# Performance work log

Measured on AMD Instinct MI355X. Metric: run time of the kernel, lower is better.

The kernel has to match this reference:

```python
import jax, jax.numpy as jnp
import numpy as np

B, N_RIGIDS, N_RES = 16, 8192, 2048
C_FRAME, C_S, N_AA = 384, 384, 21
EPS = 1e-5


def setup_inputs() -> dict:
    key = jax.random.key(0)
    ks = jax.random.split(key, 8)
    rigids_embed_flat = jax.random.normal(ks[0], (B, N_RIGIDS, C_FRAME), dtype=jnp.float32)
    rigids_to_res_idx = jax.random.randint(ks[1], (B, N_RIGIDS), 0, N_RES, dtype=jnp.int64)
    rigids_mask = jnp.ones((B, N_RIGIDS), dtype=jnp.float32)
    out = jax.random.normal(ks[2], (B, N_RES, C_S), dtype=jnp.float32)
    # params
    ln_g = jnp.ones((C_FRAME,), dtype=jnp.float32)
    ln_b = jnp.zeros((C_FRAME,), dtype=jnp.float32)
    W_su = jax.random.normal(ks[3], (C_FRAME, C_S), dtype=jnp.float32) / np.sqrt(C_FRAME)
    b_su = jnp.zeros((C_S,), dtype=jnp.float32)
    W_out = jax.random.normal(ks[4], (C_S, N_AA), dtype=jnp.float32) / np.sqrt(C_S)
    b_out = jnp.zeros((N_AA,), dtype=jnp.float32)
    return {
        "rigids_embed_flat": rigids_embed_flat,
        "rigids_to_res_idx": rigids_to_res_idx,
        "rigids_mask": rigids_mask,
        "out": out,
        "ln_g": ln_g, "ln_b": ln_b,
        "W_su": W_su, "b_su": b_su,
        "W_out": W_out, "b_out": b_out,
    }


def _layernorm(x, g, b):
    mu = jnp.mean(x, axis=-1, keepdims=True)
    var = jnp.mean(jnp.square(x - mu), axis=-1, keepdims=True)
    return (x - mu) * jax.lax.rsqrt(var + EPS) * g + b


def reference(rigids_embed_flat, rigids_to_res_idx, rigids_mask, out,
              ln_g, ln_b, W_su, b_su, W_out, b_out):
    # 1) LayerNorm over frame channel dim
    x = _layernorm(rigids_embed_flat, ln_g, ln_b)            # [B, N_rigids, c_frame]
    # 2) project frame embed -> c_s and mask invalid frames
    y = (jnp.einsum("bnf,fs->bns", x, W_su) + b_su) * rigids_mask[..., None]
    # 3) scatter-add masked frame contributions into per-residue slots
    seq_embed = jax.vmap(lambda o, yy, ii: o.at[ii].add(yy))(out, y, rigids_to_res_idx)  # [B, N_res, c_s]
    # 4) final projection to amino-acid logits
    return jnp.einsum("brs,sa->bra", seq_embed, W_out) + b_out  # [B, N_res, n_aa]
```

## Files before the change

### kernel.cpp

```cpp
#include <hip/hip_runtime.h>

#define BATCH 16
#define N_RIGIDS 8192
#define N_RES 2048
#define C_FRAME 384
#define C_S 384
#define N_AA 21
#define EPS 1e-5f

#define N_RIG_TOT (BATCH * N_RIGIDS)
#define N_ROWS    (BATCH * N_RES)
#define CAP 32
#define ZROW 32

#define GC_OFF 0
#define CS_OFF 8192
#define B2_OFF 8256
#define HIST_OFF 16384
#define ZB_OFF 65536

__global__ void __launch_bounds__(384) precompute_fused(const float* __restrict__ W_su,
                                                        const float* __restrict__ W_out,
                                                        const float* __restrict__ ln_g,
                                                        const float* __restrict__ ln_b,
                                                        const float* __restrict__ b_su,
                                                        float* __restrict__ ws) {
    __shared__ float sg[6], sb[6];
    const int a = blockIdx.x;
    const int f = threadIdx.x;
    const float4* wrow = (const float4*)(W_su + (size_t)f * C_S);
    float wc = 0.f;
    for (int j = 0; j < C_S / 4; ++j) {
        float4 v = wrow[j];
        wc += v.x * W_out[(4 * j + 0) * N_AA + a];
        wc += v.y * W_out[(4 * j + 1) * N_AA + a];
        wc += v.z * W_out[(4 * j + 2) * N_AA + a];
        wc += v.w * W_out[(4 * j + 3) * N_AA + a];
    }
    float gval = ln_g[f] * wc;
    ws[GC_OFF + f * N_AA + a] = gval;
    float bval = ln_b[f] * wc + b_su[f] * W_out[f * N_AA + a];
    float g = gval, b = bval;
#pragma unroll
    for (int off = 32; off >= 1; off >>= 1) {
        g += __shfl_xor(g, off);
        b += __shfl_xor(b, off);
    }
    int lane = f & 63, w = f >> 6;
    if (lane == 0) { sg[w] = g; sb[w] = b; }
    __syncthreads();
    if (f == 0) {
        float cs = 0.f, b2 = 0.f;
#pragma unroll
        for (int i = 0; i < 6; ++i) { cs += sg[i]; b2 += sb[i]; }
        ws[CS_OFF + a] = cs;
        ws[B2_OFF + a] = b2;
    }
}

__global__ void __launch_bounds__(128) zcompute(const float* __restrict__ embed,
                                                const int* __restrict__ idx,
                                                const float* __restrict__ mask,
                                                const float* __restrict__ ws,
                                                float* __restrict__ zb,
                                                int* __restrict__ hist) {
    __shared__ float lds[2][128 * 33];
    const int tid = threadIdx.x;
    const int t = blockIdx.x * 128 + tid;
    const float* __restrict__ Gc = ws + GC_OFF;
    const float4* gb = (const float4*)(embed + (size_t)blockIdx.x * (128 * C_FRAME));
    float4 buf[8];
    float d[N_AA];
#pragma unroll
    for (int a = 0; a < N_AA; ++a) d[a] = 0.f;
    float sum = 0.f, sumsq = 0.f;

#pragma unroll
    for (int k = 0; k < 8; ++k) {
        int f4 = tid + 128 * k;
        buf[k] = gb[(f4 >> 3) * 96 + (f4 & 7)];
    }
#pragma unroll
    for (int k = 0; k < 8; ++k) {
        int f4 = tid + 128 * k;
        float* p = &lds[0][(f4 >> 3) * 33 + (f4 & 7) * 4];
        p[0] = buf[k].x; p[1] = buf[k].y; p[2] = buf[k].z; p[3] = buf[k].w;
    }
    __syncthreads();

    for (int c = 0; c < 12; ++c) {
        if (c + 1 < 12) {
            const float4* gn = gb + (c + 1) * 8;
#pragma unroll
            for (int k = 0; k < 8; ++k) {
                int f4 = tid + 128 * k;
                buf[k] = gn[(f4 >> 3) * 96 + (f4 & 7)];
            }
        }
        const float* row = &lds[c & 1][tid * 33];
        const float* g = Gc + (c * 32) * N_AA;
#pragma unroll 4
        for (int cc = 0; cc < 32; ++cc) {
            float x = row[cc];
            sum += x; sumsq += x * x;
#pragma unroll
            for (int a = 0; a < N_AA; ++a) d[a] += x * g[cc * N_AA + a];
        }
        if (c + 1 < 12) {
#pragma unroll
            for (int k = 0; k < 8; ++k) {
                int f4 = tid + 128 * k;
                float* p = &lds[(c + 1) & 1][(f4 >> 3) * 33 + (f4 & 7) * 4];
                p[0] = buf[k].x; p[1] = buf[k].y; p[2] = buf[k].z; p[3] = buf[k].w;
            }
            __syncthreads();
        }
    }

    float mu  = sum * (1.f / C_FRAME);
    float var = sumsq * (1.f / C_FRAME) - mu * mu;
    float inv = rsqrtf(var + EPS);
    float m = mask[t];
    int res = idx[t];
    int b = t >> 13;
    int g = (b << 11) + res;
    const float* cs = ws + CS_OFF;
    const float* b2 = ws + B2_OFF;
    float v[N_AA];
#pragma unroll
    for (int a = 0; a < N_AA; ++a) v[a] = m * (inv * (d[a] - mu * cs[a]) + b2[a]);
    int slot = atomicAdd(hist + g, 1);
    if (slot < CAP) {
        float4* zr = (float4*)(zb + ((size_t)g * CAP + slot) * ZROW);
        zr[0] = make_float4(v[0], v[1], v[2], v[3]);
        zr[1] = make_float4(v[4], v[5], v[6], v[7]);
        zr[2] = make_float4(v[8], v[9], v[10], v[11]);
        zr[3] = make_float4(v[12], v[13], v[14], v[15]);
        zr[4] = make_float4(v[16], v[17], v[18], v[19]);
        ((float*)zr)[20] = v[20];
    }
}

__global__ void __launch_bounds__(128) final_gather(const float* __restrict__ out_in,
                                                    const float* __restrict__ W_out,
                                                    const float* __restrict__ b_out,
                                                    const float* __restrict__ zb,
                                                    const int* __restrict__ hist,
                                                    float* __restrict__ logits) {
    __shared__ float lds[2][128 * 33];
    const int tid = threadIdx.x;
    const int gidx = blockIdx.x * 128 + tid;
    const float4* gb = (const float4*)(out_in + (size_t)blockIdx.x * (128 * C_S));
    float4 buf[8];
    float acc[N_AA];
#pragma unroll
    for (int a = 0; a < N_AA; ++a) acc[a] = b_out[a];

#pragma unroll
    for (int k = 0; k < 8; ++k) {
        int f4 = tid + 128 * k;
        buf[k] = gb[(f4 >> 3) * 96 + (f4 & 7)];
    }
#pragma unroll
    for (int k = 0; k < 8; ++k) {
        int f4 = tid + 128 * k;
        float* p = &lds[0][(f4 >> 3) * 33 + (f4 & 7) * 4];
        p[0] = buf[k].x; p[1] = buf[k].y; p[2] = buf[k].z; p[3] = buf[k].w;
    }
    __syncthreads();

    for (int c = 0; c < 12; ++c) {
        if (c + 1 < 12) {
            const float4* gn = gb + (c + 1) * 8;
#pragma unroll
            for (int k = 0; k < 8; ++k) {
                int f4 = tid + 128 * k;
                buf[k] = gn[(f4 >> 3) * 96 + (f4 & 7)];
            }
        }
        const float* row = &lds[c & 1][tid * 33];
        const float* w = W_out + (c * 32) * N_AA;
#pragma unroll 4
        for (int cc = 0; cc < 32; ++cc) {
            float x = row[cc];
#pragma unroll
            for (int a = 0; a < N_AA; ++a) acc[a] += x * w[cc * N_AA + a];
        }
        if (c + 1 < 12) {
#pragma unroll
            for (int k = 0; k < 8; ++k) {
                int f4 = tid + 128 * k;
                float* p = &lds[(c + 1) & 1][(f4 >> 3) * 33 + (f4 & 7) * 4];
                p[0] = buf[k].x; p[1] = buf[k].y; p[2] = buf[k].z; p[3] = buf[k].w;
            }
            __syncthreads();
        }
    }

    int cnt = hist[gidx];
    if (cnt > CAP) cnt = CAP;
    const float* zbase = zb + (size_t)gidx * CAP * ZROW;
    for (int i = 0; i < cnt; ++i) {
        const float4* zr = (const float4*)(zbase + i * ZROW);
        float4 z0 = zr[0], z1 = zr[1], z2 = zr[2], z3 = zr[3], z4 = zr[4];
        float  z5 = ((const float*)zr)[20];
        acc[0] += z0.x; acc[1] += z0.y; acc[2] += z0.z; acc[3] += z0.w;
        acc[4] += z1.x; acc[5] += z1.y; acc[6] += z1.z; acc[7] += z1.w;
        acc[8] += z2.x; acc[9] += z2.y; acc[10] += z2.z; acc[11] += z2.w;
        acc[12] += z3.x; acc[13] += z3.y; acc[14] += z3.z; acc[15] += z3.w;
        acc[16] += z4.x; acc[17] += z4.y; acc[18] += z4.z; acc[19] += z4.w;
        acc[20] += z5;
    }
    float* o = logits + (size_t)gidx * N_AA;
#pragma unroll
    for (int a = 0; a < N_AA; ++a) o[a] = acc[a];
}

extern "C" void kernel_launch(void* const* d_in, const int* in_sizes, int n_in,
                              void* d_out, int out_size, void* d_ws, size_t ws_size,
                              hipStream_t stream) {
    const float* embed  = (const float*)d_in[0];
    const int*   idx    = (const int*)d_in[1];
    const float* mask   = (const float*)d_in[2];
    const float* out_in = (const float*)d_in[3];
    const float* ln_g   = (const float*)d_in[4];
    const float* ln_b   = (const float*)d_in[5];
    const float* W_su   = (const float*)d_in[6];
    const float* b_su   = (const float*)d_in[7];
    const float* W_out  = (const float*)d_in[8];
    const float* b_out  = (const float*)d_in[9];
    float* logits = (float*)d_out;
    float* ws = (float*)d_ws;
    float* zb   = ws + ZB_OFF;
    int*   hist = (int*)(ws + HIST_OFF);

    hipMemsetAsync(hist, 0, N_ROWS * sizeof(int), stream);
    hipLaunchKernelGGL(precompute_fused, dim3(N_AA), dim3(384), 0, stream,
                       W_su, W_out, ln_g, ln_b, b_su, ws);
    hipLaunchKernelGGL(zcompute, dim3(N_RIG_TOT / 128), dim3(128), 0, stream,
                       embed, idx, mask, ws, zb, hist);
    hipLaunchKernelGGL(final_gather, dim3(N_ROWS / 128), dim3(128), 0, stream,
                       out_in, W_out, b_out, zb, hist, logits);
}
```

Measured before the change: 429.8 us.

## Split final_gather rows across four threads and pad W_out for vector loads

The final gather kernel now assigns four threads per residue row, each handling a quarter of the channel chunk, and combines partial sums with lane shuffles. Blocks now cover 32 rows instead of 128, so there are four times as many. W_out is copied into a 24-wide padded layout in the workspace so the inner loop can load it as float4. The precompute kernel is also split into 64-thread blocks that combine partial sums with atomics, which needs an extra memset. The aim is more parallelism and occupancy in the final stage, at the cost of shuffle reductions and a strided gather of the scatter buffer.

```diff
diff --git a/kernel.cpp b/kernel.cpp
--- a/kernel.cpp
+++ b/kernel.cpp
@@ -6,6 +6,7 @@
 #define C_FRAME 384
 #define C_S 384
 #define N_AA 21
+#define N_AA_PAD 24
 #define EPS 1e-5f
 
 #define N_RIG_TOT (BATCH * N_RIGIDS)
@@ -16,18 +17,26 @@
 #define GC_OFF 0
 #define CS_OFF 8192
 #define B2_OFF 8256
-#define HIST_OFF 16384
+#define WP_OFF 8320
+#define HIST_OFF 18432
 #define ZB_OFF 65536
 
-__global__ void __launch_bounds__(384) precompute_fused(const float* __restrict__ W_su,
-                                                        const float* __restrict__ W_out,
-                                                        const float* __restrict__ ln_g,
-                                                        const float* __restrict__ ln_b,
-                                                        const float* __restrict__ b_su,
-                                                        float* __restrict__ ws) {
-    __shared__ float sg[6], sb[6];
-    const int a = blockIdx.x;
-    const int f = threadIdx.x;
+__global__ void __launch_bounds__(64) precompute_fused(const float* __restrict__ W_su,
+                                                       const float* __restrict__ W_out,
+                                                       const float* __restrict__ ln_g,
+                                                       const float* __restrict__ ln_b,
+                                                       const float* __restrict__ b_su,
+                                                       float* __restrict__ ws) {
+    const int f = blockIdx.x * 64 + threadIdx.x;
+    if (blockIdx.y == N_AA) {
+        float* wp = ws + WP_OFF + (size_t)f * N_AA_PAD;
+        const float* wo = W_out + (size_t)f * N_AA;
+#pragma unroll
+        for (int a = 0; a < N_AA; ++a) wp[a] = wo[a];
+        wp[21] = 0.f; wp[22] = 0.f; wp[23] = 0.f;
+        return;
+    }
+    const int a = blockIdx.y;
     const float4* wrow = (const float4*)(W_su + (size_t)f * C_S);
     float wc = 0.f;
     for (int j = 0; j < C_S / 4; ++j) {
@@ -46,15 +55,9 @@
         g += __shfl_xor(g, off);
         b += __shfl_xor(b, off);
     }
-    int lane = f & 63, w = f >> 6;
-    if (lane == 0) { sg[w] = g; sb[w] = b; }
-    __syncthreads();
-    if (f == 0) {
-        float cs = 0.f, b2 = 0.f;
-#pragma unroll
-        for (int i = 0; i < 6; ++i) { cs += sg[i]; b2 += sb[i]; }
-        ws[CS_OFF + a] = cs;
-        ws[B2_OFF + a] = b2;
+    if (threadIdx.x == 0) {
+        atomicAdd(ws + CS_OFF + a, g);
+        atomicAdd(ws + B2_OFF + a, b);
     }
 }
 
@@ -142,27 +145,30 @@
 }
 
 __global__ void __launch_bounds__(128) final_gather(const float* __restrict__ out_in,
-                                                    const float* __restrict__ W_out,
                                                     const float* __restrict__ b_out,
+                                                    const float* __restrict__ ws,
                                                     const float* __restrict__ zb,
                                                     const int* __restrict__ hist,
                                                     float* __restrict__ logits) {
-    __shared__ float lds[2][128 * 33];
+    __shared__ float lds[2][32 * 33];
     const int tid = threadIdx.x;
-    const int gidx = blockIdx.x * 128 + tid;
-    const float4* gb = (const float4*)(out_in + (size_t)blockIdx.x * (128 * C_S));
-    float4 buf[8];
-    float acc[N_AA];
-#pragma unroll
-    for (int a = 0; a < N_AA; ++a) acc[a] = b_out[a];
-
-#pragma unroll
-    for (int k = 0; k < 8; ++k) {
+    const int r = tid >> 2;
+    const int ks = tid & 3;
+    const int gidx = blockIdx.x * 32 + r;
+    const float* __restrict__ Wp = ws + WP_OFF;
+    const float4* gb = (const float4*)(out_in + (size_t)blockIdx.x * (32 * C_S));
+    float4 buf[2];
+    float acc[N_AA_PAD];
+#pragma unroll
+    for (int a = 0; a < N_AA_PAD; ++a) acc[a] = 0.f;
+
+#pragma unroll
+    for (int k = 0; k < 2; ++k) {
         int f4 = tid + 128 * k;
         buf[k] = gb[(f4 >> 3) * 96 + (f4 & 7)];
     }
 #pragma unroll
-    for (int k = 0; k < 8; ++k) {
+    for (int k = 0; k < 2; ++k) {
         int f4 = tid + 128 * k;
         float* p = &lds[0][(f4 >> 3) * 33 + (f4 & 7) * 4];
         p[0] = buf[k].x; p[1] = buf[k].y; p[2] = buf[k].z; p[3] = buf[k].w;
@@ -173,22 +179,28 @@
         if (c + 1 < 12) {
             const float4* gn = gb + (c + 1) * 8;
 #pragma unroll
-            for (int k = 0; k < 8; ++k) {
+            for (int k = 0; k < 2; ++k) {
                 int f4 = tid + 128 * k;
                 buf[k] = gn[(f4 >> 3) * 96 + (f4 & 7)];
             }
         }
-        const float* row = &lds[c & 1][tid * 33];
-        const float* w = W_out + (c * 32) * N_AA;
-#pragma unroll 4
-        for (int cc = 0; cc < 32; ++cc) {
+        const float* row = &lds[c & 1][r * 33 + ks * 8];
+        const float4* w4 = (const float4*)(Wp + (size_t)(c * 32 + ks * 8) * N_AA_PAD);
+#pragma unroll
+        for (int cc = 0; cc < 8; ++cc) {
             float x = row[cc];
 #pragma unroll
-            for (int a = 0; a < N_AA; ++a) acc[a] += x * w[cc * N_AA + a];
-        }
-        if (c + 1 < 12) {
-#pragma unroll
-            for (int k = 0; k < 8; ++k) {
+            for (int q = 0; q < 6; ++q) {
+                float4 wv = w4[cc * 6 + q];
+                acc[4 * q + 0] += x * wv.x;
+                acc[4 * q + 1] += x * wv.y;
+                acc[4 * q + 2] += x * wv.z;
+                acc[4 * q + 3] += x * wv.w;
+            }
+        }
+        if (c + 1 < 12) {
+#pragma unroll
+            for (int k = 0; k < 2; ++k) {
                 int f4 = tid + 128 * k;
                 float* p = &lds[(c + 1) & 1][(f4 >> 3) * 33 + (f4 & 7) * 4];
                 p[0] = buf[k].x; p[1] = buf[k].y; p[2] = buf[k].z; p[3] = buf[k].w;
@@ -200,20 +212,16 @@
     int cnt = hist[gidx];
     if (cnt > CAP) cnt = CAP;
     const float* zbase = zb + (size_t)gidx * CAP * ZROW;
-    for (int i = 0; i < cnt; ++i) {
-        const float4* zr = (const float4*)(zbase + i * ZROW);
-        float4 z0 = zr[0], z1 = zr[1], z2 = zr[2], z3 = zr[3], z4 = zr[4];
-        float  z5 = ((const float*)zr)[20];
-        acc[0] += z0.x; acc[1] += z0.y; acc[2] += z0.z; acc[3] += z0.w;
-        acc[4] += z1.x; acc[5] += z1.y; acc[6] += z1.z; acc[7] += z1.w;
-        acc[8] += z2.x; acc[9] += z2.y; acc[10] += z2.z; acc[11] += z2.w;
-        acc[12] += z3.x; acc[13] += z3.y; acc[14] += z3.z; acc[15] += z3.w;
-        acc[16] += z4.x; acc[17] += z4.y; acc[18] += z4.z; acc[19] += z4.w;
-        acc[20] += z5;
-    }
     float* o = logits + (size_t)gidx * N_AA;
 #pragma unroll
-    for (int a = 0; a < N_AA; ++a) o[a] = acc[a];
+    for (int a = 0; a < N_AA; ++a) {
+        float t = acc[a];
+        if (ks == 0) t += b_out[a];
+        for (int i = ks; i < cnt; i += 4) t += zbase[i * ZROW + a];
+        t += __shfl_xor(t, 1);
+        t += __shfl_xor(t, 2);
+        if (ks == 0) o[a] = t;
+    }
 }
 
 extern "C" void kernel_launch(void* const* d_in, const int* in_sizes, int n_in,
@@ -235,10 +243,11 @@
     int*   hist = (int*)(ws + HIST_OFF);
 
     hipMemsetAsync(hist, 0, N_ROWS * sizeof(int), stream);
-    hipLaunchKernelGGL(precompute_fused, dim3(N_AA), dim3(384), 0, stream,
+    hipMemsetAsync(ws + CS_OFF, 0, (B2_OFF - CS_OFF + N_AA) * sizeof(float), stream);
+    hipLaunchKernelGGL(precompute_fused, dim3(6, N_AA + 1), dim3(64), 0, stream,
                        W_su, W_out, ln_g, ln_b, b_su, ws);
     hipLaunchKernelGGL(zcompute, dim3(N_RIG_TOT / 128), dim3(128), 0, stream,
                        embed, idx, mask, ws, zb, hist);
-    hipLaunchKernelGGL(final_gather, dim3(N_ROWS / 128), dim3(128), 0, stream,
-                       out_in, W_out, b_out, zb, hist, logits);
-}
+    hipLaunchKernelGGL(final_gather, dim3(N_ROWS / 32), dim3(128), 0, stream,
+                       out_in, b_out, ws, zb, hist, logits);
+}
```

After: 499.3 us. +16.2%, slower.

## Split final_gather channel reduction across waves and parallelize precompute over blocks

Applied to the files above, without the earlier changes.

final_gather now assigns 64 rows per block and has four waves each handle a quarter of the c_s channels, reducing partial logits through LDS. The scatter-bucket gather is then spread over four threads per row, each covering a strided subset of output columns. precompute_fused spreads each amino-acid column over six 64-thread blocks and combines the partial sums with atomics into a zero-initialized buffer. This raises parallelism in both kernels, at the cost of an extra memset, float atomics and more barriers, and with fewer rows per block the number of blocks doubles.

```diff
diff --git a/kernel.cpp b/kernel.cpp
--- a/kernel.cpp
+++ b/kernel.cpp
@@ -16,18 +16,17 @@
 #define GC_OFF 0
 #define CS_OFF 8192
 #define B2_OFF 8256
-#define HIST_OFF 16384
+#define HIST_OFF 18432
 #define ZB_OFF 65536
 
-__global__ void __launch_bounds__(384) precompute_fused(const float* __restrict__ W_su,
-                                                        const float* __restrict__ W_out,
-                                                        const float* __restrict__ ln_g,
-                                                        const float* __restrict__ ln_b,
-                                                        const float* __restrict__ b_su,
-                                                        float* __restrict__ ws) {
-    __shared__ float sg[6], sb[6];
-    const int a = blockIdx.x;
-    const int f = threadIdx.x;
+__global__ void __launch_bounds__(64) precompute_fused(const float* __restrict__ W_su,
+                                                       const float* __restrict__ W_out,
+                                                       const float* __restrict__ ln_g,
+                                                       const float* __restrict__ ln_b,
+                                                       const float* __restrict__ b_su,
+                                                       float* __restrict__ ws) {
+    const int f = blockIdx.x * 64 + threadIdx.x;
+    const int a = blockIdx.y;
     const float4* wrow = (const float4*)(W_su + (size_t)f * C_S);
     float wc = 0.f;
     for (int j = 0; j < C_S / 4; ++j) {
@@ -46,15 +45,9 @@
         g += __shfl_xor(g, off);
         b += __shfl_xor(b, off);
     }
-    int lane = f & 63, w = f >> 6;
-    if (lane == 0) { sg[w] = g; sb[w] = b; }
-    __syncthreads();
-    if (f == 0) {
-        float cs = 0.f, b2 = 0.f;
-#pragma unroll
-        for (int i = 0; i < 6; ++i) { cs += sg[i]; b2 += sb[i]; }
-        ws[CS_OFF + a] = cs;
-        ws[B2_OFF + a] = b2;
+    if (threadIdx.x == 0) {
+        atomicAdd(ws + CS_OFF + a, g);
+        atomicAdd(ws + B2_OFF + a, b);
     }
 }
 
@@ -141,79 +134,86 @@
     }
 }
 
-__global__ void __launch_bounds__(128) final_gather(const float* __restrict__ out_in,
+__global__ void __launch_bounds__(256) final_gather(const float* __restrict__ out_in,
                                                     const float* __restrict__ W_out,
                                                     const float* __restrict__ b_out,
                                                     const float* __restrict__ zb,
                                                     const int* __restrict__ hist,
                                                     float* __restrict__ logits) {
-    __shared__ float lds[2][128 * 33];
+    __shared__ float lds[4][64 * 33];
     const int tid = threadIdx.x;
-    const int gidx = blockIdx.x * 128 + tid;
-    const float4* gb = (const float4*)(out_in + (size_t)blockIdx.x * (128 * C_S));
+    const int w = tid >> 6;
+    const int l = tid & 63;
+    const float4* gb = (const float4*)(out_in + (size_t)blockIdx.x * (64 * C_S));
     float4 buf[8];
     float acc[N_AA];
 #pragma unroll
-    for (int a = 0; a < N_AA; ++a) acc[a] = b_out[a];
-
-#pragma unroll
-    for (int k = 0; k < 8; ++k) {
-        int f4 = tid + 128 * k;
-        buf[k] = gb[(f4 >> 3) * 96 + (f4 & 7)];
-    }
-#pragma unroll
-    for (int k = 0; k < 8; ++k) {
-        int f4 = tid + 128 * k;
-        float* p = &lds[0][(f4 >> 3) * 33 + (f4 & 7) * 4];
+    for (int a = 0; a < N_AA; ++a) acc[a] = 0.f;
+
+#pragma unroll
+    for (int k = 0; k < 8; ++k) {
+        int f4 = l + 64 * k;
+        buf[k] = gb[(f4 >> 3) * 96 + w * 8 + (f4 & 7)];
+    }
+#pragma unroll
+    for (int k = 0; k < 8; ++k) {
+        int f4 = l + 64 * k;
+        float* p = &lds[w][(f4 >> 3) * 33 + (f4 & 7) * 4];
         p[0] = buf[k].x; p[1] = buf[k].y; p[2] = buf[k].z; p[3] = buf[k].w;
     }
     __syncthreads();
 
-    for (int c = 0; c < 12; ++c) {
-        if (c + 1 < 12) {
-            const float4* gn = gb + (c + 1) * 8;
-#pragma unroll
-            for (int k = 0; k < 8; ++k) {
-                int f4 = tid + 128 * k;
-                buf[k] = gn[(f4 >> 3) * 96 + (f4 & 7)];
-            }
-        }
-        const float* row = &lds[c & 1][tid * 33];
-        const float* w = W_out + (c * 32) * N_AA;
+    for (int j = 0; j < 3; ++j) {
+        const int c = w + 4 * j;
+        if (j < 2) {
+            const int cn = c + 4;
+#pragma unroll
+            for (int k = 0; k < 8; ++k) {
+                int f4 = l + 64 * k;
+                buf[k] = gb[(f4 >> 3) * 96 + cn * 8 + (f4 & 7)];
+            }
+        }
+        const float* srow = &lds[w][l * 33];
+        const float* g = W_out + (size_t)(c * 32) * N_AA;
 #pragma unroll 4
         for (int cc = 0; cc < 32; ++cc) {
-            float x = row[cc];
-#pragma unroll
-            for (int a = 0; a < N_AA; ++a) acc[a] += x * w[cc * N_AA + a];
-        }
-        if (c + 1 < 12) {
-#pragma unroll
-            for (int k = 0; k < 8; ++k) {
-                int f4 = tid + 128 * k;
-                float* p = &lds[(c + 1) & 1][(f4 >> 3) * 33 + (f4 & 7) * 4];
+            float x = srow[cc];
+#pragma unroll
+            for (int a = 0; a < N_AA; ++a) acc[a] += x * g[cc * N_AA + a];
+        }
+        if (j < 2) {
+            __syncthreads();
+#pragma unroll
+            for (int k = 0; k < 8; ++k) {
+                int f4 = l + 64 * k;
+                float* p = &lds[w][(f4 >> 3) * 33 + (f4 & 7) * 4];
                 p[0] = buf[k].x; p[1] = buf[k].y; p[2] = buf[k].z; p[3] = buf[k].w;
             }
             __syncthreads();
         }
     }
 
+    __syncthreads();
+    float* red = (float*)lds;
+    float* myred = red + ((size_t)w * 64 + l) * 22;
+#pragma unroll
+    for (int a = 0; a < N_AA; ++a) myred[a] = acc[a];
+    __syncthreads();
+
+    const int r = tid >> 2;
+    const int jj = tid & 3;
+    const int gidx = blockIdx.x * 64 + r;
     int cnt = hist[gidx];
     if (cnt > CAP) cnt = CAP;
     const float* zbase = zb + (size_t)gidx * CAP * ZROW;
-    for (int i = 0; i < cnt; ++i) {
-        const float4* zr = (const float4*)(zbase + i * ZROW);
-        float4 z0 = zr[0], z1 = zr[1], z2 = zr[2], z3 = zr[3], z4 = zr[4];
-        float  z5 = ((const float*)zr)[20];
-        acc[0] += z0.x; acc[1] += z0.y; acc[2] += z0.z; acc[3] += z0.w;
-        acc[4] += z1.x; acc[5] += z1.y; acc[6] += z1.z; acc[7] += z1.w;
-        acc[8] += z2.x; acc[9] += z2.y; acc[10] += z2.z; acc[11] += z2.w;
-        acc[12] += z3.x; acc[13] += z3.y; acc[14] += z3.z; acc[15] += z3.w;
-        acc[16] += z4.x; acc[17] += z4.y; acc[18] += z4.z; acc[19] += z4.w;
-        acc[20] += z5;
-    }
     float* o = logits + (size_t)gidx * N_AA;
-#pragma unroll
-    for (int a = 0; a < N_AA; ++a) o[a] = acc[a];
+    for (int a = jj; a < N_AA; a += 4) {
+        float t4 = b_out[a]
+                 + red[(0 * 64 + r) * 22 + a] + red[(1 * 64 + r) * 22 + a]
+                 + red[(2 * 64 + r) * 22 + a] + red[(3 * 64 + r) * 22 + a];
+        for (int i = 0; i < cnt; ++i) t4 += zbase[i * ZROW + a];
+        o[a] = t4;
+    }
 }
 
 extern "C" void kernel_launch(void* const* d_in, const int* in_sizes, int n_in,
@@ -235,10 +235,11 @@
     int*   hist = (int*)(ws + HIST_OFF);
 
     hipMemsetAsync(hist, 0, N_ROWS * sizeof(int), stream);
-    hipLaunchKernelGGL(precompute_fused, dim3(N_AA), dim3(384), 0, stream,
+    hipMemsetAsync(ws + CS_OFF, 0, (B2_OFF - CS_OFF + N_AA) * sizeof(float), stream);
+    hipLaunchKernelGGL(precompute_fused, dim3(6, N_AA), dim3(64), 0, stream,
                        W_su, W_out, ln_g, ln_b, b_su, ws);
     hipLaunchKernelGGL(zcompute, dim3(N_RIG_TOT / 128), dim3(128), 0, stream,
                        embed, idx, mask, ws, zb, hist);
-    hipLaunchKernelGGL(final_gather, dim3(N_ROWS / 128), dim3(128), 0, stream,
+    hipLaunchKernelGGL(final_gather, dim3(N_ROWS / 64), dim3(256), 0, stream,
                        out_in, W_out, b_out, zb, hist, logits);
 }
```

After: 430.4 us. Within noise of the previous version (+0.2%).
